# Performance work log

Hardware: AMD Instinct MI355X
Metric: run time of the kernel (lower is better)

The kernel has to match this reference:

```python
import jax, jax.numpy as jnp
import numpy as np

B, S, Hd = 4, 2048, 1024
NH, D = 16, 64

def setup_inputs() -> dict:
    key = jax.random.key(0)
    ks = jax.random.split(key, 8)
    scale = 0.02
    return {
        "hidden_states": jax.random.normal(ks[0], (B, S, Hd), dtype=jnp.float32),
        "attention_mask": jnp.zeros((B, 1, 1, S), dtype=jnp.float32),
        "relations": jax.random.normal(ks[1], (1, 1, S, D), dtype=jnp.float32),
        "Wq": jax.random.normal(ks[2], (Hd, Hd), dtype=jnp.float32) * scale,
        "bq": jnp.zeros((Hd,), dtype=jnp.float32),
        "Wk": jax.random.normal(ks[3], (Hd, Hd), dtype=jnp.float32) * scale,
        "bk": jnp.zeros((Hd,), dtype=jnp.float32),
        "Wv": jax.random.normal(ks[4], (Hd, Hd), dtype=jnp.float32) * scale,
        "bv": jnp.zeros((Hd,), dtype=jnp.float32),
    }

def _heads(x):  # [B,S,Hd] -> [B,NH,S,D]
    return x.reshape(x.shape[0], x.shape[1], NH, D).transpose(0, 2, 1, 3)

def _rotate_half_interleaved(x):
    # stack([-x_odd, x_even], -1).reshape_as(x)
    return jnp.stack([-x[..., 1::2], x[..., ::2]], axis=-1).reshape(x.shape)

def reference(hidden_states, attention_mask, relations, Wq, bq, Wk, bk, Wv, bv):
    q = _heads(hidden_states @ Wq.T + bq)
    k = _heads(hidden_states @ Wk.T + bk)
    v = _heads(hidden_states @ Wv.T + bv)

    # interleaved rotary: cos from odd slots, sin from even slots, each repeated x2
    cos_pos = jnp.repeat(relations[..., 1::2], 2, axis=-1)  # [1,1,S,D]
    sin_pos = jnp.repeat(relations[..., ::2], 2, axis=-1)
    q = q * cos_pos + _rotate_half_interleaved(q) * sin_pos
    k = k * cos_pos + _rotate_half_interleaved(k) * sin_pos

    scores = jnp.einsum("bhqd,bhkd->bhqk", q, k) / jnp.sqrt(jnp.float32(D))
    scores = scores + attention_mask
    probs = jax.nn.softmax(scores, axis=-1)
    ctx = jnp.einsum("bhqk,bhkd->bhqd", probs, v)
    return ctx.transpose(0, 2, 1, 3).reshape(hidden_states.shape[0], hidden_states.shape[1], NH * D)
```

## Files before the change

### kernel.cpp

```cpp
#include <hip/hip_runtime.h>

typedef __attribute__((ext_vector_type(8))) short short8;
typedef __attribute__((ext_vector_type(4))) float f32x4;
typedef __attribute__((ext_vector_type(4))) unsigned int u32x4;
typedef __attribute__((ext_vector_type(2))) unsigned int u32x2;
typedef __attribute__((ext_vector_type(4))) unsigned short u16x4;

#define NHEADS 16
#define DHEAD 64
#define SEQ 2048
#define BATCH 4
#define HD 1024
#define MTOT 8192

static __device__ __forceinline__ unsigned short f2b(float x) {
  unsigned u = __builtin_bit_cast(unsigned, x);
  u += 0x7fffu + ((u >> 16) & 1u);
  return (unsigned short)(u >> 16);
}

static __device__ __forceinline__ unsigned pk2h(float lo, float hi) {
  unsigned a = __builtin_bit_cast(unsigned, lo) + 0x8000u;
  unsigned b = __builtin_bit_cast(unsigned, hi) + 0x8000u;
  return (a >> 16) | (b & 0xffff0000u);
}

static __device__ __forceinline__ void gll16(const void* g, void* l) {
  __builtin_amdgcn_global_load_lds(
      (const __attribute__((address_space(1))) unsigned int*)g,
      (__attribute__((address_space(3))) unsigned int*)l, 16, 0, 0);
}

__global__ void cvt_bf16(const float* __restrict__ src,
                         unsigned short* __restrict__ dst, int n4) {
  int i = blockIdx.x * blockDim.x + threadIdx.x;
  if (i < n4) {
    f32x4 v = ((const f32x4*)src)[i];
    u16x4 o;
    o[0] = f2b(v[0]); o[1] = f2b(v[1]); o[2] = f2b(v[2]); o[3] = f2b(v[3]);
    ((u16x4*)dst)[i] = o;
  }
}

#define WQ4 (HD * HD / 4)
__global__ void prep(const float* __restrict__ Wq, const float* __restrict__ Wk,
                     const float* __restrict__ Wv, const float* __restrict__ mask,
                     unsigned short* __restrict__ Wb,
                     unsigned short* __restrict__ Wm) {
  int i = blockIdx.x * blockDim.x + threadIdx.x;
  if (i < 3 * WQ4) {
    int rg = i / WQ4;
    int idx = i - rg * WQ4;
    const float* src = (rg == 0) ? Wq : (rg == 1) ? Wk : Wv;
    f32x4 v = ((const f32x4*)src)[idx];
    u16x4 o;
    o[0] = f2b(v[0]); o[1] = f2b(v[1]); o[2] = f2b(v[2]); o[3] = f2b(v[3]);
    ((u16x4*)(Wb + (size_t)rg * HD * HD))[idx] = o;
  } else {
    int j = i - 3 * WQ4;
    f32x4 v = ((const f32x4*)mask)[j];
    u16x4 o;
    o[0] = f2b(__expf(v[0])); o[1] = f2b(__expf(v[1]));
    o[2] = f2b(__expf(v[2])); o[3] = f2b(__expf(v[3]));
    ((u16x4*)Wm)[j] = o;
  }
}

__global__ __launch_bounds__(256) void qkv_gemm(
    const unsigned short* __restrict__ X,
    const unsigned short* __restrict__ Wall,
    const float* __restrict__ bq, const float* __restrict__ bk,
    const float* __restrict__ bv,
    const float* __restrict__ rel,
    const float* __restrict__ mask,
    unsigned short* __restrict__ Qo,
    unsigned short* __restrict__ Ko,
    unsigned short* __restrict__ Vt) {
  __shared__ __align__(16) unsigned short As[2][128 * 64];
  __shared__ __align__(16) unsigned short Bs[2][128 * 64];

  const int t = threadIdx.x;
  const int lane = t & 63;
  const int w = t >> 6;

  const int n = blockIdx.x;
  const int xcd = n & 7;
  const int li = n >> 3;
  const int bx = xcd * 8 + (li & 7);
  const int pp = li >> 3;
  const int by = pp & 7;
  const int bz = pp >> 3;

  const unsigned short* W = Wall + (size_t)bz * HD * HD;
  const int m0 = bx * 128;
  const int n0 = by * 128;

  f32x4 acc[4][4];
  for (int i = 0; i < 4; i++)
    for (int j = 0; j < 4; j++) acc[i][j] = (f32x4){0.f, 0.f, 0.f, 0.f};

  const int wm = (w & 1) * 64;
  const int wn = (w >> 1) * 64;
  const int cl = lane & 15;
  const int qd = lane >> 4;

  auto stage = [&](int bi, int k0) {
#pragma unroll
    for (int j = 0; j < 4; j++) {
      int r0 = w * 32 + j * 8;
      int r = r0 + (lane >> 3);
      int cg = (((lane & 7) ^ (r & 7)) << 3);
      gll16(X + (size_t)(m0 + r) * HD + k0 + cg, &As[bi][r0 * 64]);
      gll16(W + (size_t)(n0 + r) * HD + k0 + cg, &Bs[bi][r0 * 64]);
    }
  };

  stage(0, 0);

#pragma unroll 1
  for (int kt = 0; kt < HD / 64; kt++) {
    const int bi = kt & 1;
    __syncthreads();
    if (kt + 1 < HD / 64) stage(bi ^ 1, (kt + 1) * 64);
    const unsigned short* Asb = &As[bi][0];
    const unsigned short* Bsb = &Bs[bi][0];

#pragma unroll
    for (int ks = 0; ks < 2; ks++) {
      const int cc = ks * 4 + qd;
      short8 af[4], bf[4];
#pragma unroll
      for (int i = 0; i < 4; i++) {
        int r = wm + i * 16 + cl;
        af[i] = *(const short8*)(Asb + r * 64 + ((cc ^ (r & 7)) << 3));
      }
#pragma unroll
      for (int j = 0; j < 4; j++) {
        int r = wn + j * 16 + cl;
        bf[j] = *(const short8*)(Bsb + r * 64 + ((cc ^ (r & 7)) << 3));
      }
      if (bz < 2) {
#pragma unroll
        for (int i = 0; i < 4; i++)
#pragma unroll
          for (int j = 0; j < 4; j++)
            acc[i][j] = __builtin_amdgcn_mfma_f32_16x16x32_bf16(bf[j], af[i],
                                                                acc[i][j], 0, 0, 0);
      } else {
#pragma unroll
        for (int i = 0; i < 4; i++)
#pragma unroll
          for (int j = 0; j < 4; j++)
            acc[i][j] = __builtin_amdgcn_mfma_f32_16x16x32_bf16(af[i], bf[j],
                                                                acc[i][j], 0, 0, 0);
      }
    }
  }

  if (bz == 2) {
    const int hh = (n0 + wn) >> 6;
#pragma unroll
    for (int i = 0; i < 4; i++) {
      int mb = m0 + wm + i * 16 + qd * 4;
      int bb = mb >> 11, ssb = mb & (SEQ - 1);
      f32x4 mk = *(const f32x4*)(mask + bb * SEQ + ssb);
      f32x4 w4;
#pragma unroll
      for (int r = 0; r < 4; r++) w4[r] = __expf(mk[r]);
      int colp = (ssb & ~31) | ((ssb & 12) << 1) | (((ssb >> 4) & 1) << 2);
#pragma unroll
      for (int j = 0; j < 4; j++) {
        int nn = n0 + wn + j * 16 + cl;
        int dd = j * 16 + cl;
        float bn = bv[nn];
        u32x2 pk;
        pk[0] = pk2h((acc[i][j][0] + bn) * w4[0], (acc[i][j][1] + bn) * w4[1]);
        pk[1] = pk2h((acc[i][j][2] + bn) * w4[2], (acc[i][j][3] + bn) * w4[3]);
        *(u32x2*)(Vt + ((size_t)((bb * NHEADS + hh) * DHEAD + dd)) * SEQ + colp) = pk;
      }
    }
  } else {
    const float* bias = (bz == 0) ? bq : bk;
    unsigned short* Out = (bz == 0) ? Qo : Ko;
    const float qs = (bz == 0) ? 0.125f * 1.4426950408889634f : 1.0f;
    const int hh = (n0 + wn) >> 6;
#pragma unroll
    for (int j = 0; j < 4; j++) {
      int nb = n0 + wn + j * 16 + qd * 4;
      f32x4 b4 = *(const f32x4*)(bias + nb);
      int ddb = j * 16 + qd * 4;
#pragma unroll
      for (int i = 0; i < 4; i++) {
        int s = m0 + wm + i * 16 + cl;
        int bb = s >> 11, ss = s & (SEQ - 1);
        f32x4 rl = *(const f32x4*)(rel + ss * DHEAD + ddb);
        float x0 = acc[i][j][0] + b4[0];
        float x1 = acc[i][j][1] + b4[1];
        float x2 = acc[i][j][2] + b4[2];
        float x3 = acc[i][j][3] + b4[3];
        float y0 = (x0 * rl[1] - x1 * rl[0]) * qs;
        float y1 = (x1 * rl[1] + x0 * rl[0]) * qs;
        float y2 = (x2 * rl[3] - x3 * rl[2]) * qs;
        float y3 = (x3 * rl[3] + x2 * rl[2]) * qs;
        u32x2 pk;
        pk[0] = pk2h(y0, y1);
        pk[1] = pk2h(y2, y3);
        *(u32x2*)(Out + (((size_t)(bb * NHEADS + hh)) * SEQ + ss) * DHEAD + ddb) = pk;
      }
    }
  }
}

__global__ __launch_bounds__(256, 2) void attn(
    const unsigned short* __restrict__ Q,
    const unsigned short* __restrict__ K,
    const unsigned short* __restrict__ Vt,
    const unsigned short* __restrict__ wmask,
    float* __restrict__ out) {
  __shared__ __align__(16) unsigned short Ks[2][128 * 64];
  __shared__ __align__(16) unsigned short Vs[2][64 * 128];

  const int t = threadIdx.x;
  const int lane = t & 63;
  const int w = t >> 6;

  const int n = blockIdx.x;
  const int xcd = n & 7;
  const int li = n >> 3;
  const int bh = xcd * 8 + (li >> 4);
  const int qt = li & 15;

  const int b = bh >> 4, h = bh & 15;
  const int s0 = qt * 128;
  const unsigned short* Qp = Q + (size_t)bh * SEQ * DHEAD;
  const unsigned short* Kp = K + (size_t)bh * SEQ * DHEAD;
  const unsigned short* Vp = Vt + (size_t)bh * DHEAD * SEQ;
  const unsigned short* wmp = wmask + b * SEQ;

  const int cl = lane & 15;
  const int qd = lane >> 4;

  short8 qf[2][2];
#pragma unroll
  for (int mt = 0; mt < 2; mt++)
#pragma unroll
    for (int ks = 0; ks < 2; ks++)
      qf[mt][ks] = *(const short8*)(Qp + (size_t)(s0 + w * 32 + mt * 16 + cl) * DHEAD +
                                    ks * 32 + qd * 8);

  f32x4 ov[2][4];
  f32x4 ovl[2];
#pragma unroll
  for (int mt = 0; mt < 2; mt++) {
    ovl[mt] = (f32x4){0.f, 0.f, 0.f, 0.f};
#pragma unroll
    for (int dt = 0; dt < 4; dt++) ov[mt][dt] = (f32x4){0.f, 0.f, 0.f, 0.f};
  }

  auto stage = [&](int bi, int kt) {
#pragma unroll
    for (int j = 0; j < 4; j++) {
      int r0 = w * 32 + j * 8;
      int r = r0 + (lane >> 3);
      int c = (lane & 7) ^ (r & 7);
      gll16(Kp + (size_t)(kt + r) * DHEAD + c * 8, &Ks[bi][r0 * 64]);
    }
#pragma unroll
    for (int j = 0; j < 4; j++) {
      int r0 = w * 16 + j * 4;
      int r = r0 + (lane >> 4);
      int c = (lane & 15) ^ (r & 7);
      gll16(Vp + (size_t)r * SEQ + kt + c * 8, &Vs[bi][r0 * 128]);
    }
  };

  stage(0, 0);

  for (int it = 0; it < SEQ / 128; it++) {
    const int kt = it * 128;
    const int bi = it & 1;
    __syncthreads();
    if (it + 1 < SEQ / 128) stage(1 - bi, kt + 128);
    const unsigned short* Ksb = &Ks[bi][0];
    const unsigned short* Vsb = &Vs[bi][0];

    short8 wf[4];
#pragma unroll
    for (int c = 0; c < 4; c++) {
      u32x2 w0 = *(const u32x2*)(wmp + kt + c * 32 + qd * 4);
      u32x2 w1 = *(const u32x2*)(wmp + kt + c * 32 + 16 + qd * 4);
      u32x4 ww = {w0[0], w0[1], w1[0], w1[1]};
      wf[c] = __builtin_bit_cast(short8, ww);
    }

    f32x4 sc[2][8];
#pragma unroll
    for (int mt = 0; mt < 2; mt++)
#pragma unroll
      for (int nt = 0; nt < 8; nt++) sc[mt][nt] = (f32x4){0.f, 0.f, 0.f, 0.f};
#pragma unroll
    for (int ks = 0; ks < 2; ks++) {
#pragma unroll
      for (int nt = 0; nt < 8; nt++) {
        int krow = nt * 16 + cl;
        short8 kf = *(const short8*)(Ksb + krow * 64 +
                                     (((ks * 4 + qd) ^ (krow & 7)) << 3));
        sc[0][nt] = __builtin_amdgcn_mfma_f32_16x16x32_bf16(kf, qf[0][ks], sc[0][nt], 0, 0, 0);
        sc[1][nt] = __builtin_amdgcn_mfma_f32_16x16x32_bf16(kf, qf[1][ks], sc[1][nt], 0, 0, 0);
      }
    }

    unsigned pw[2][8][2];
#pragma unroll
    for (int mt = 0; mt < 2; mt++) {
#pragma unroll
      for (int nt = 0; nt < 8; nt++) {
        float p0 = __builtin_amdgcn_exp2f(sc[mt][nt][0]);
        float p1 = __builtin_amdgcn_exp2f(sc[mt][nt][1]);
        float p2 = __builtin_amdgcn_exp2f(sc[mt][nt][2]);
        float p3 = __builtin_amdgcn_exp2f(sc[mt][nt][3]);
        pw[mt][nt][0] = pk2h(p0, p1);
        pw[mt][nt][1] = pk2h(p2, p3);
      }
    }

#pragma unroll
    for (int c = 0; c < 4; c++) {
      u32x4 bb0 = {pw[0][2 * c][0], pw[0][2 * c][1], pw[0][2 * c + 1][0], pw[0][2 * c + 1][1]};
      u32x4 bb1 = {pw[1][2 * c][0], pw[1][2 * c][1], pw[1][2 * c + 1][0], pw[1][2 * c + 1][1]};
      short8 bf0 = __builtin_bit_cast(short8, bb0);
      short8 bf1 = __builtin_bit_cast(short8, bb1);
      ovl[0] = __builtin_amdgcn_mfma_f32_16x16x32_bf16(wf[c], bf0, ovl[0], 0, 0, 0);
      ovl[1] = __builtin_amdgcn_mfma_f32_16x16x32_bf16(wf[c], bf1, ovl[1], 0, 0, 0);
#pragma unroll
      for (int dt = 0; dt < 4; dt++) {
        int vrow = dt * 16 + cl;
        short8 vf = *(const short8*)(Vsb + vrow * 128 +
                                     (((c * 4 + qd) ^ (vrow & 7)) << 3));
        ov[0][dt] = __builtin_amdgcn_mfma_f32_16x16x32_bf16(vf, bf0, ov[0][dt], 0, 0, 0);
        ov[1][dt] = __builtin_amdgcn_mfma_f32_16x16x32_bf16(vf, bf1, ov[1][dt], 0, 0, 0);
      }
    }
  }

#pragma unroll
  for (int mt = 0; mt < 2; mt++) {
    float rl = 1.0f / ovl[mt][0];
    int s = s0 + w * 32 + mt * 16 + cl;
    float* ob = out + ((size_t)b * SEQ + s) * HD + h * DHEAD;
#pragma unroll
    for (int dt = 0; dt < 4; dt++) {
      f32x4 o;
      o[0] = ov[mt][dt][0] * rl;
      o[1] = ov[mt][dt][1] * rl;
      o[2] = ov[mt][dt][2] * rl;
      o[3] = ov[mt][dt][3] * rl;
      *(f32x4*)(ob + dt * 16 + qd * 4) = o;
    }
  }
}

extern "C" void kernel_launch(void* const* d_in, const int* in_sizes, int n_in,
                              void* d_out, int out_size, void* d_ws, size_t ws_size,
                              hipStream_t stream) {
  const float* hidden = (const float*)d_in[0];
  const float* mask   = (const float*)d_in[1];
  const float* rel    = (const float*)d_in[2];
  const float* Wq     = (const float*)d_in[3];
  const float* bq     = (const float*)d_in[4];
  const float* Wk     = (const float*)d_in[5];
  const float* bk     = (const float*)d_in[6];
  const float* Wv     = (const float*)d_in[7];
  const float* bv     = (const float*)d_in[8];
  float* out = (float*)d_out;

  unsigned short* Xb = (unsigned short*)d_ws;
  unsigned short* Wb = Xb + (size_t)MTOT * HD;
  unsigned short* Qb = Wb + (size_t)3 * HD * HD;
  unsigned short* Kb = Qb + (size_t)MTOT * HD;
  unsigned short* Vb = Kb + (size_t)MTOT * HD;
  unsigned short* Wm = Vb + (size_t)MTOT * HD;

  {
    int n4 = MTOT * HD / 4;
    cvt_bf16<<<n4 / 256, 256, 0, stream>>>(hidden, Xb, n4);
  }
  prep<<<(3 * WQ4 + BATCH * SEQ / 4) / 256, 256, 0, stream>>>(Wq, Wk, Wv, mask, Wb, Wm);
  qkv_gemm<<<dim3(1536), 256, 0, stream>>>(Xb, Wb, bq, bk, bv, rel, mask, Qb, Kb, Vb);
  attn<<<dim3(1024), 256, 0, stream>>>(Qb, Kb, Vb, Wm, out);
}
```

Measured before the change: 304.5 us.

## Restructure QKV GEMM into split-phase pipelined loads with 128x32 warp tiles

Each warp in the QKV projection GEMM now computes a 128x32 tile instead of a 64x64 quadrant. Global-to-LDS staging is split into two halves per K-step, synchronised with explicit vmcnt waits and barriers so later loads overlap the first half of the MFMA work. The MFMA sections also raise wave priority with setprio. This is meant to hide memory latency better, at the cost of more A-fragment LDS reads per warp, more complex sync, and a wasted redundant prefetch on the last iteration.

```diff
diff --git a/kernel.cpp b/kernel.cpp
--- a/kernel.cpp
+++ b/kernel.cpp
@@ -91,77 +91,138 @@
   const int by = pp & 7;
   const int bz = pp >> 3;
 
-  const unsigned short* W = Wall + (size_t)bz * HD * HD;
+  const unsigned short* Wp = Wall + (size_t)bz * HD * HD;
   const int m0 = bx * 128;
   const int n0 = by * 128;
 
-  f32x4 acc[4][4];
-  for (int i = 0; i < 4; i++)
-    for (int j = 0; j < 4; j++) acc[i][j] = (f32x4){0.f, 0.f, 0.f, 0.f};
-
-  const int wm = (w & 1) * 64;
-  const int wn = (w >> 1) * 64;
   const int cl = lane & 15;
   const int qd = lane >> 4;
 
-  auto stage = [&](int bi, int k0) {
-#pragma unroll
-    for (int j = 0; j < 4; j++) {
-      int r0 = w * 32 + j * 8;
-      int r = r0 + (lane >> 3);
-      int cg = (((lane & 7) ^ (r & 7)) << 3);
-      gll16(X + (size_t)(m0 + r) * HD + k0 + cg, &As[bi][r0 * 64]);
-      gll16(W + (size_t)(n0 + r) * HD + k0 + cg, &Bs[bi][r0 * 64]);
-    }
+  f32x4 acc[8][2];
+#pragma unroll
+  for (int i = 0; i < 8; i++)
+#pragma unroll
+    for (int j = 0; j < 2; j++) acc[i][j] = (f32x4){0.f, 0.f, 0.f, 0.f};
+
+  auto stageA = [&](int b, int q, int k0) {
+    int rr = (q << 5) + (t >> 3);
+    gll16(X + (size_t)(m0 + rr) * HD + k0 + (((t & 7) ^ (rr & 7)) << 3),
+          &As[b][((q << 5) + (w << 3)) * 64]);
   };
-
-  stage(0, 0);
+  auto stageB = [&](int b, int q, int k0) {
+    int rr = (q << 5) + (t >> 3);
+    gll16(Wp + (size_t)(n0 + rr) * HD + k0 + (((t & 7) ^ (rr & 7)) << 3),
+          &Bs[b][((q << 5) + (w << 3)) * 64]);
+  };
+
+#define SYNC(N)                               \
+  __builtin_amdgcn_sched_barrier(0);          \
+  asm volatile("s_waitcnt vmcnt(" #N ")");    \
+  __builtin_amdgcn_sched_barrier(0);          \
+  __builtin_amdgcn_s_barrier();               \
+  __builtin_amdgcn_sched_barrier(0);
+
+  stageA(0, 0, 0); stageA(0, 1, 0);
+  stageB(0, 0, 0); stageB(0, 1, 0);
+  stageB(0, 2, 0); stageB(0, 3, 0);
+  stageA(0, 2, 0); stageA(0, 3, 0);
 
 #pragma unroll 1
-  for (int kt = 0; kt < HD / 64; kt++) {
-    const int bi = kt & 1;
-    __syncthreads();
-    if (kt + 1 < HD / 64) stage(bi ^ 1, (kt + 1) * 64);
+  for (int it = 0; it < 16; it++) {
+    const int bi = it & 1;
+    const int nb = bi ^ 1;
+    const int kn = ((it + 1) * 64) & 1023;
     const unsigned short* Asb = &As[bi][0];
     const unsigned short* Bsb = &Bs[bi][0];
 
-#pragma unroll
-    for (int ks = 0; ks < 2; ks++) {
-      const int cc = ks * 4 + qd;
-      short8 af[4], bf[4];
-#pragma unroll
-      for (int i = 0; i < 4; i++) {
-        int r = wm + i * 16 + cl;
-        af[i] = *(const short8*)(Asb + r * 64 + ((cc ^ (r & 7)) << 3));
-      }
-#pragma unroll
-      for (int j = 0; j < 4; j++) {
-        int r = wn + j * 16 + cl;
-        bf[j] = *(const short8*)(Bsb + r * 64 + ((cc ^ (r & 7)) << 3));
-      }
-      if (bz < 2) {
-#pragma unroll
-        for (int i = 0; i < 4; i++)
-#pragma unroll
-          for (int j = 0; j < 4; j++)
-            acc[i][j] = __builtin_amdgcn_mfma_f32_16x16x32_bf16(bf[j], af[i],
-                                                                acc[i][j], 0, 0, 0);
-      } else {
-#pragma unroll
-        for (int i = 0; i < 4; i++)
-#pragma unroll
-          for (int j = 0; j < 4; j++)
-            acc[i][j] = __builtin_amdgcn_mfma_f32_16x16x32_bf16(af[i], bf[j],
-                                                                acc[i][j], 0, 0, 0);
-      }
-    }
-  }
+    SYNC(2);
+
+    stageA(nb, 0, kn); stageA(nb, 1, kn);
+    stageB(nb, 0, kn); stageB(nb, 1, kn);
+
+    short8 bf[2][2];
+#pragma unroll
+    for (int j = 0; j < 2; j++) {
+      int r = w * 32 + j * 16 + cl;
+      const unsigned short* rp = &Bsb[r * 64];
+#pragma unroll
+      for (int ks = 0; ks < 2; ks++)
+        bf[j][ks] = *(const short8*)(rp + (((ks * 4 + qd) ^ (r & 7)) << 3));
+    }
+
+    __builtin_amdgcn_s_setprio(1);
+#pragma unroll
+    for (int mq = 0; mq < 2; mq++) {
+#pragma unroll
+      for (int ks = 0; ks < 2; ks++) {
+        short8 af[2];
+#pragma unroll
+        for (int i = 0; i < 2; i++) {
+          int r = mq * 32 + i * 16 + cl;
+          af[i] = *(const short8*)(&Asb[r * 64] +
+                                   (((ks * 4 + qd) ^ (r & 7)) << 3));
+        }
+        if (bz < 2) {
+#pragma unroll
+          for (int i = 0; i < 2; i++)
+#pragma unroll
+            for (int j = 0; j < 2; j++)
+              acc[mq * 2 + i][j] = __builtin_amdgcn_mfma_f32_16x16x32_bf16(
+                  bf[j][ks], af[i], acc[mq * 2 + i][j], 0, 0, 0);
+        } else {
+#pragma unroll
+          for (int i = 0; i < 2; i++)
+#pragma unroll
+            for (int j = 0; j < 2; j++)
+              acc[mq * 2 + i][j] = __builtin_amdgcn_mfma_f32_16x16x32_bf16(
+                  af[i], bf[j][ks], acc[mq * 2 + i][j], 0, 0, 0);
+        }
+      }
+    }
+    __builtin_amdgcn_s_setprio(0);
+
+    SYNC(4);
+
+    stageB(nb, 2, kn); stageB(nb, 3, kn);
+    stageA(nb, 2, kn); stageA(nb, 3, kn);
+
+    __builtin_amdgcn_s_setprio(1);
+#pragma unroll
+    for (int mq = 2; mq < 4; mq++) {
+#pragma unroll
+      for (int ks = 0; ks < 2; ks++) {
+        short8 af[2];
+#pragma unroll
+        for (int i = 0; i < 2; i++) {
+          int r = mq * 32 + i * 16 + cl;
+          af[i] = *(const short8*)(&Asb[r * 64] +
+                                   (((ks * 4 + qd) ^ (r & 7)) << 3));
+        }
+        if (bz < 2) {
+#pragma unroll
+          for (int i = 0; i < 2; i++)
+#pragma unroll
+            for (int j = 0; j < 2; j++)
+              acc[mq * 2 + i][j] = __builtin_amdgcn_mfma_f32_16x16x32_bf16(
+                  bf[j][ks], af[i], acc[mq * 2 + i][j], 0, 0, 0);
+        } else {
+#pragma unroll
+          for (int i = 0; i < 2; i++)
+#pragma unroll
+            for (int j = 0; j < 2; j++)
+              acc[mq * 2 + i][j] = __builtin_amdgcn_mfma_f32_16x16x32_bf16(
+                  af[i], bf[j][ks], acc[mq * 2 + i][j], 0, 0, 0);
+        }
+      }
+    }
+    __builtin_amdgcn_s_setprio(0);
+  }
+#undef SYNC
 
   if (bz == 2) {
-    const int hh = (n0 + wn) >> 6;
-#pragma unroll
-    for (int i = 0; i < 4; i++) {
-      int mb = m0 + wm + i * 16 + qd * 4;
+#pragma unroll
+    for (int mf = 0; mf < 8; mf++) {
+      int mb = m0 + mf * 16 + qd * 4;
       int bb = mb >> 11, ssb = mb & (SEQ - 1);
       f32x4 mk = *(const f32x4*)(mask + bb * SEQ + ssb);
       f32x4 w4;
@@ -169,13 +230,14 @@
       for (int r = 0; r < 4; r++) w4[r] = __expf(mk[r]);
       int colp = (ssb & ~31) | ((ssb & 12) << 1) | (((ssb >> 4) & 1) << 2);
 #pragma unroll
-      for (int j = 0; j < 4; j++) {
-        int nn = n0 + wn + j * 16 + cl;
-        int dd = j * 16 + cl;
-        float bn = bv[nn];
+      for (int nf = 0; nf < 2; nf++) {
+        int feat = n0 + w * 32 + nf * 16 + cl;
+        int hh = feat >> 6;
+        int dd = feat & 63;
+        float bn = bv[feat];
         u32x2 pk;
-        pk[0] = pk2h((acc[i][j][0] + bn) * w4[0], (acc[i][j][1] + bn) * w4[1]);
-        pk[1] = pk2h((acc[i][j][2] + bn) * w4[2], (acc[i][j][3] + bn) * w4[3]);
+        pk[0] = pk2h((acc[mf][nf][0] + bn) * w4[0], (acc[mf][nf][1] + bn) * w4[1]);
+        pk[1] = pk2h((acc[mf][nf][2] + bn) * w4[2], (acc[mf][nf][3] + bn) * w4[3]);
         *(u32x2*)(Vt + ((size_t)((bb * NHEADS + hh) * DHEAD + dd)) * SEQ + colp) = pk;
       }
     }
@@ -183,21 +245,21 @@
     const float* bias = (bz == 0) ? bq : bk;
     unsigned short* Out = (bz == 0) ? Qo : Ko;
     const float qs = (bz == 0) ? 0.125f * 1.4426950408889634f : 1.0f;
-    const int hh = (n0 + wn) >> 6;
-#pragma unroll
-    for (int j = 0; j < 4; j++) {
-      int nb = n0 + wn + j * 16 + qd * 4;
-      f32x4 b4 = *(const f32x4*)(bias + nb);
-      int ddb = j * 16 + qd * 4;
-#pragma unroll
-      for (int i = 0; i < 4; i++) {
-        int s = m0 + wm + i * 16 + cl;
+#pragma unroll
+    for (int nf = 0; nf < 2; nf++) {
+      int feat0 = n0 + w * 32 + nf * 16 + qd * 4;
+      int hh = feat0 >> 6;
+      int ddb = feat0 & 63;
+      f32x4 b4 = *(const f32x4*)(bias + feat0);
+#pragma unroll
+      for (int mf = 0; mf < 8; mf++) {
+        int s = m0 + mf * 16 + cl;
         int bb = s >> 11, ss = s & (SEQ - 1);
         f32x4 rl = *(const f32x4*)(rel + ss * DHEAD + ddb);
-        float x0 = acc[i][j][0] + b4[0];
-        float x1 = acc[i][j][1] + b4[1];
-        float x2 = acc[i][j][2] + b4[2];
-        float x3 = acc[i][j][3] + b4[3];
+        float x0 = acc[mf][nf][0] + b4[0];
+        float x1 = acc[mf][nf][1] + b4[1];
+        float x2 = acc[mf][nf][2] + b4[2];
+        float x3 = acc[mf][nf][3] + b4[3];
         float y0 = (x0 * rl[1] - x1 * rl[0]) * qs;
         float y1 = (x1 * rl[1] + x0 * rl[0]) * qs;
         float y2 = (x2 * rl[3] - x3 * rl[2]) * qs;
```

New measurement: 276.0 us. -9.4%, faster.
